# Optimization experiments

Hardware: AMD Instinct MI355X
Metric: run time of the kernel (lower is better)

The kernel has to match this reference:

```python
import jax, jax.numpy as jnp
import numpy as np
from jax import lax

FI, FO, K, EPS = 512, 256, 3, 1e-06


def _fir_kernel(gain):
    f = jnp.array([1.0, 3.0, 3.0, 1.0], dtype=jnp.float32)
    f = f[None, :] * f[:, None]
    f = f / f.sum() * gain  # (4,4), symmetric so conv-vs-correlation flip is a no-op
    return f


def setup_inputs() -> dict:
    key = jax.random.key(0)
    k1, k2 = jax.random.split(key)
    x = jax.random.normal(k1, (8, FI, 64, 64), dtype=jnp.float32)
    w = jax.random.normal(k2, (1, FO, FI, K, K), dtype=jnp.float32)
    return {"x": x, "w": w}


def reference(x, w):
    w_scale = (FI * K * K) ** (-0.5)
    wm = w[0] * w_scale  # (fo, fi, k, k); per-sample scale is constant across batch
    demod = lax.rsqrt(jnp.sum(wm * wm, axis=(1, 2, 3)) + EPS)  # (fo,)
    wm = wm * demod[:, None, None, None]
    # torch conv_transpose2d(stride=2, padding=0) with weight (fi, fo, k, k) where
    # weight[i, o] = wm[o, i]  ==  dilated conv with kernel flip(wm) OIHW, pad k-1=2.
    kern = wm[:, :, ::-1, ::-1]
    y = lax.conv_general_dilated(
        x, kern, window_strides=(1, 1), padding=[(2, 2), (2, 2)],
        lhs_dilation=(2, 2), dimension_numbers=("NCHW", "OIHW", "NCHW"))
    # upFirDn2D with scale=2, conv_k=3: p=0 -> pad (1,1) both dims, filter gain 4
    f = _fir_kernel(4.0)
    C = y.shape[1]
    fk = jnp.broadcast_to(f[None, None], (C, 1, 4, 4))
    y = lax.conv_general_dilated(
        y, fk, window_strides=(1, 1), padding=[(1, 1), (1, 1)],
        feature_group_count=C, dimension_numbers=("NCHW", "OIHW", "NCHW"))
    return y  # (8, 256, 128, 128)
```

## Files before the change

kernel.cpp:

```cpp
#include <hip/hip_runtime.h>

typedef unsigned short u16;
typedef unsigned int u32;
typedef __attribute__((ext_vector_type(8))) short bf16x8;
typedef __attribute__((ext_vector_type(4))) float f32x4;

#define XP_BYTES 35684352
#define YB_BYTES 68714544
#define HY_OFF   (XP_BYTES + YB_BYTES)
#define WS_NEED  ((size_t)HY_OFF + 2359296)
#define CS 16776

__device__ inline u16 f2bf(float f) {
  union { float f; unsigned u; } v; v.f = f;
  unsigned r = v.u + 0x7fffu + ((v.u >> 16) & 1u);
  return (u16)(r >> 16);
}

__device__ inline void gl_lds16(const u16* g, u16* l) {
  __builtin_amdgcn_global_load_lds(
      (const __attribute__((address_space(1))) unsigned int*)g,
      (__attribute__((address_space(3))) unsigned int*)l, 16, 0, 0);
}

__global__ void xprep(const float* __restrict__ x, u16* __restrict__ xp) {
  __shared__ float tile[64 * 65];
  int bid = blockIdx.x;
  int cc = bid & 7, h = (bid >> 3) & 63, n = bid >> 9;
  int c0 = cc * 64;
  int t = threadIdx.x;
  const float* xb = x + ((size_t)(n * 512 + c0) * 64 + h) * 64;
  for (int r = 0; r < 16; ++r) {
    int flat = r * 256 + t;
    int ci = flat >> 6, w = flat & 63;
    tile[w * 65 + ci] = xb[(size_t)ci * 4096 + w];
  }
  __syncthreads();
  for (int r = 0; r < 8; ++r) {
    int flat = r * 256 + t;
    int pr = flat & 31;
    int w = flat >> 5;
    int ci = pr * 2;
    float v0 = tile[w * 65 + ci], v1 = tile[w * 65 + ci + 1];
    unsigned pk = (unsigned)f2bf(v0) | ((unsigned)f2bf(v1) << 16);
    int kcabs = cc * 2 + (ci >> 5);
    int chl = ci & 31;
    u16* dst = xp + (size_t)(n * 16 + kcabs) * 139392 +
               (size_t)((h + 1) * 66 + (w + 1)) * 32 + chl;
    *(unsigned*)dst = pk;
  }
  if (t < 64) {
    int seg = t >> 4;
    int colsel = (seg >> 1) ? 65 : 0;
    int pl = cc * 2 + (seg & 1);
    int ui = t & 15;
    u16* dst = xp + (size_t)(n * 16 + pl) * 139392 +
               (size_t)((h + 1) * 66 + colsel) * 32 + ui * 2;
    *(u32*)dst = 0u;
  }
  if (h == 0 || h == 63) {
    int rowbase = (h == 0) ? 0 : 65 * 66;
    for (int j = t; j < 2112; j += 256) {
      int seg = j >> 4;
      int ui = j & 15;
      int pl = cc * 2 + (seg & 1);
      int pos = seg >> 1;
      u16* dst = xp + (size_t)(n * 16 + pl) * 139392 +
                 (size_t)(rowbase + pos) * 32 + ui * 2;
      *(u32*)dst = 0u;
    }
  }
}

__global__ void wprep9(const float* __restrict__ w, u16* __restrict__ Hy) {
  __shared__ float wl[4608];
  __shared__ float red[256];
  int o = blockIdx.x, t = threadIdx.x;
  const float* wo = w + (size_t)o * 4608;
  float s = 0.f;
  for (int j = t; j < 4608; j += 256) { float v = wo[j]; wl[j] = v; s += v * v; }
  red[t] = s;
  __syncthreads();
  for (int st = 128; st; st >>= 1) { if (t < st) red[t] += red[t + st]; __syncthreads(); }
  float demod = rsqrtf(red[0] * (1.0f / 4608.0f) + 1e-6f);
  float scale = demod * 0.014731391274719739f;
  const int DY[9] = {0, 2, 0, 2, 0, 2, 1, 1, 1};
  const int DX[9] = {0, 0, 2, 2, 1, 1, 0, 2, 1};
  for (int i = t; i < 512; i += 256) {
    int kc = i >> 5, il = i & 31;
#pragma unroll
    for (int pl = 0; pl < 9; ++pl) {
      float g = wl[i * 9 + DY[pl] * 3 + DX[pl]] * scale;
      Hy[(size_t)(pl * 16 + kc) * 8192 + (size_t)o * 32 + il] = f2bf(g);
    }
  }
}

#define BARR() __builtin_amdgcn_s_barrier()
#define WAITL() do { asm volatile("s_waitcnt lgkmcnt(0)" ::: "memory"); __builtin_amdgcn_sched_barrier(0); } while (0)
#define WAITV1() do { asm volatile("s_waitcnt vmcnt(1)" ::: "memory"); __builtin_amdgcn_sched_barrier(0); } while (0)
#define WAITV0() do { asm volatile("s_waitcnt vmcnt(0)" ::: "memory"); __builtin_amdgcn_sched_barrier(0); } while (0)

__device__ __forceinline__ void rdA4(const u16* sbA, int la, int grp, int hi,
                                     bf16x8 af[4]) {
#pragma unroll
  for (int ti = 0; ti < 4; ++ti) {
    int p = ti * 16 + la;
    int slot = (hi * 4 + grp) ^ (p & 7);
    af[ti] = *(const bf16x8*)(sbA + p * 64 + slot * 8);
  }
}

__device__ __forceinline__ bf16x8 rdB1(const u16* sb, int r, int grp) {
  int p = r & 63, hi = r >> 6;
  int slot = (hi * 4 + grp) ^ (p & 7);
  return *(const bf16x8*)(sb + 8192 + p * 64 + slot * 8);
}

template <int MI, int NI>
__device__ __forceinline__ void qmfma4(const bf16x8 af[4], bf16x8 bf,
                                       f32x4 acc[8][2]) {
#pragma unroll
  for (int ti = 0; ti < 4; ++ti)
    acc[MI * 4 + ti][NI] = __builtin_amdgcn_mfma_f32_16x16x32_bf16(
        af[ti], bf, acc[MI * 4 + ti][NI], 0, 0, 0);
}

__device__ __forceinline__ void stA1(const u16* __restrict__ xp, u16* d,
                                     int tile, int NK, u32 a,
                                     u32 adj1, u32 adj2, u32 adj3) {
  if (tile < NK) {
    int tap = tile >> 4;
    u32 ko = (u32)((tile & 15) * 139392);
    u32 adj = tap == 0 ? 0u : (tap == 1 ? adj1 : (tap == 2 ? adj2 : adj3));
    gl_lds16(xp + (a + ko - adj), d);
  }
}

__device__ __forceinline__ void stB1(const u16* __restrict__ hb, u16* d,
                                     int tile, int NK, u32 b) {
  if (tile < NK) {
    int tap = tile >> 4;
    u32 ko = (u32)(tap * 131072 + (tile & 15) * 8192);
    gl_lds16(hb + (b + ko), d);
  }
}

__global__ __launch_bounds__(512, 4) void conv_y(const u16* __restrict__ xp,
                                                 const u16* __restrict__ Hy,
                                                 u16* __restrict__ yb) {
  __shared__ __align__(16) u16 su[24576];

  int bid = blockIdx.x;
  int t = threadIdx.x;
  int wid = t >> 6, lane = t & 63;

  int img = bid & 7;
  int kk = bid >> 3;
  int mt, oh, Wp, CNT, NTAP, PB, PO, STLIM;
  u32 adj1 = 0, adj2 = 0, adj3 = 0;
  if (kk < 34)       { int k2 = kk;       mt = k2 >> 1; oh = k2 & 1; Wp = 66; CNT = 4290; NTAP = 4; PB = 0; PO = 0;     STLIM = 4296;
                       adj1 = 2112u; adj2 = 32u; adj3 = 2144u; }
  else if (kk < 68)  { int k2 = kk - 34;  mt = k2 >> 1; oh = k2 & 1; Wp = 64; CNT = 4160; NTAP = 2; PB = 4; PO = 4296;  STLIM = 4160;
                       adj1 = 2112u; }
  else if (kk < 102) { int k2 = kk - 68;  mt = k2 >> 1; oh = k2 & 1; Wp = 66; CNT = 4224; NTAP = 2; PB = 6; PO = 8456;  STLIM = 4224;
                       adj1 = 32u; }
  else               { int k2 = kk - 102; mt = k2 >> 1; oh = k2 & 1; Wp = 64; CNT = 4096; NTAP = 1; PB = 8; PO = 12680; STLIM = 4096; }

  int m0 = mt * 256;
  int o0 = oh * 128;
  int NK = NTAP * 16;
  int NITER = NTAP * 8;
  const u16* hb = Hy + (size_t)PB * 131072;

  int wm = wid >> 2, wn = wid & 3;
  int la = lane & 15, grp = lane >> 4;

  int sp = t >> 3;
  int se = (t & 7) ^ (sp & 7);
  int shi = se >> 2, sc = se & 3;
  int sloc = shi * 64 + sp;

  u32 gA0, gA1, gB;
  {
    u32 ib = (u32)img * 2230272u;
    int m = m0 + sloc;
    if (m > CNT - 1) m = CNT - 1;
    u32 a = (u32)m / (u32)Wp;
    u32 b = (u32)m - a * (u32)Wp;
    gA0 = ib + ((a + 1) * 66 + (b + 1)) * 32 + sc * 8;
    m = m0 + 128 + sloc;
    if (m > CNT - 1) m = CNT - 1;
    a = (u32)m / (u32)Wp;
    b = (u32)m - a * (u32)Wp;
    gA1 = ib + ((a + 1) * 66 + (b + 1)) * 32 + sc * 8;
    gB = (u32)((o0 + sloc) * 32 + sc * 8);
  }
  int ws = wid * 512;

  f32x4 acc[8][2];
#pragma unroll
  for (int i = 0; i < 8; ++i)
#pragma unroll
    for (int j = 0; j < 2; ++j) acc[i][j] = (f32x4){0.f, 0.f, 0.f, 0.f};

  stB1(hb, su + 8192 + ws, 0, NK, gB);
  stA1(xp, su + 0 + ws, 0, NK, gA0, adj1, adj2, adj3);
  stA1(xp, su + 4096 + ws, 0, NK, gA1, adj1, adj2, adj3);
  stB1(hb, su + 20480 + ws, 1, NK, gB);
  WAITV1();
  BARR();

  bf16x8 af[4], bf0, bf1;

#pragma unroll 1
  for (int it = 0; it < NITER; ++it) {
    int t0 = 2 * it;
    bool more = (it + 1 < NITER);

    rdA4(su + wm * 4096, la, grp, 0, af);
    bf0 = rdB1(su, wn * 32 + la, grp);
    stA1(xp, su + 12288 + ws, t0 + 1, NK, gA0, adj1, adj2, adj3);
    BARR(); WAITL();
    __builtin_amdgcn_s_setprio(1); qmfma4<0, 0>(af, bf0, acc); __builtin_amdgcn_s_setprio(0);
    BARR();
    bf1 = rdB1(su, wn * 32 + 16 + la, grp);
    stA1(xp, su + 16384 + ws, t0 + 1, NK, gA1, adj1, adj2, adj3);
    BARR(); WAITL();
    __builtin_amdgcn_s_setprio(1); qmfma4<0, 1>(af, bf1, acc); __builtin_amdgcn_s_setprio(0);
    BARR();
    rdA4(su + wm * 4096, la, grp, 1, af);
    stB1(hb, su + 8192 + ws, t0 + 2, NK, gB);
    BARR(); WAITL();
    __builtin_amdgcn_s_setprio(1);
    qmfma4<1, 1>(af, bf1, acc); qmfma4<1, 0>(af, bf0, acc);
    __builtin_amdgcn_s_setprio(0);
    if (more) { WAITV1(); } else { WAITV0(); }
    BARR();
    rdA4(su + 12288 + wm * 4096, la, grp, 0, af);
    bf0 = rdB1(su + 12288, wn * 32 + la, grp);
    stA1(xp, su + 0 + ws, t0 + 2, NK, gA0, adj1, adj2, adj3);
    BARR(); WAITL();
    __builtin_amdgcn_s_setprio(1); qmfma4<0, 0>(af, bf0, acc); __builtin_amdgcn_s_setprio(0);
    BARR();
    bf1 = rdB1(su + 12288, wn * 32 + 16 + la, grp);
    stA1(xp, su + 4096 + ws, t0 + 2, NK, gA1, adj1, adj2, adj3);
    BARR(); WAITL();
    __builtin_amdgcn_s_setprio(1); qmfma4<0, 1>(af, bf1, acc); __builtin_amdgcn_s_setprio(0);
    BARR();
    rdA4(su + 12288 + wm * 4096, la, grp, 1, af);
    stB1(hb, su + 20480 + ws, t0 + 3, NK, gB);
    BARR(); WAITL();
    __builtin_amdgcn_s_setprio(1);
    qmfma4<1, 1>(af, bf1, acc); qmfma4<1, 0>(af, bf0, acc);
    __builtin_amdgcn_s_setprio(0);
    if (more) { WAITV1(); }
    BARR();
  }

  WAITV0();
  __syncthreads();
  u16* ybp = yb + 8;
#pragma unroll 1
  for (int r = 0; r < 2; ++r) {
    if ((wn >> 1) == r) {
      int base_orl = (wn & 1) * 32;
#pragma unroll
      for (int nj = 0; nj < 2; ++nj) {
        int orl = base_orl + nj * 16 + la;
        int x7 = orl & 7;
#pragma unroll
        for (int mi8 = 0; mi8 < 8; ++mi8)
#pragma unroll
          for (int jp = 0; jp < 2; ++jp) {
            int ml = wm * 128 + mi8 * 16 + grp * 4 + jp * 2;
            u32 pk = (u32)f2bf(acc[mi8][nj][jp * 2]) |
                     ((u32)f2bf(acc[mi8][nj][jp * 2 + 1]) << 16);
            *(u32*)(su + orl * 256 + (((ml >> 3) ^ x7) * 8) + (ml & 7)) = pk;
          }
      }
    }
    __syncthreads();
    {
      int ol = t >> 3, s2 = t & 7;
      int og = o0 + r * 64 + ol;
      size_t gb = (size_t)(img * 256 + og) * CS + PO + m0;
      int x7 = ol & 7;
#pragma unroll
      for (int i = 0; i < 4; ++i) {
        int cidx = s2 * 4 + i;
        int m = cidx * 8;
        if (m0 + m < STLIM)
          *(bf16x8*)(ybp + gb + m) = *(const bf16x8*)(su + ol * 256 + ((cidx ^ x7) * 8));
      }
    }
    if (r == 0) __syncthreads();
  }
}

__global__ void fir2(const u16* __restrict__ yb, float* __restrict__ z) {
  int flat = blockIdx.x * 256 + threadIdx.x;
  int qh = flat & 15, phb = (flat >> 4) & 31, o = (flat >> 9) & 255, n = flat >> 17;
  const u16* cb = yb + 8 + (size_t)(n * 256 + o) * CS;
  int a0 = 2 * phb - 1;
  int b0 = 4 * qh - 1;

  float out[4][8];
#pragma unroll
  for (int i = 0; i < 4; ++i)
#pragma unroll
    for (int j = 0; j < 8; ++j) out[i][j] = 0.f;

  const int PO_[4] = {0, 4296, 8456, 12680};
  const int WP_[4] = {66, 64, 66, 64};
  const int HA_[4] = {65, 65, 64, 64};
  const int WB_[4] = {65, 64, 65, 64};

#pragma unroll
  for (int ph = 0; ph < 4; ++ph) {
    int rp = ph >> 1, rq = ph & 1;
    const u16* pb = cb + PO_[ph];
    float hcol[4][8];
#pragma unroll
    for (int la = 0; la < 4; ++la) {
      if (rp == 0 && la == 0) continue;
      int ag = a0 + la;
      bool rv = (ag >= 0) && (ag < HA_[ph]);
      const u16* rb = pb + (ag * WP_[ph] + b0 - 1);
      u32 ls[4];
      ls[0] = *(const u32*)(rb);
      ls[1] = *(const u32*)(rb + 2);
      ls[2] = *(const u32*)(rb + 4);
      ls[3] = *(const u32*)(rb + 6);
      float v[6];
#pragma unroll
      for (int lb = 0; lb < 6; ++lb) {
        int jj = lb + 1;
        u32 w16 = (jj & 1) ? (ls[jj >> 1] >> 16) : (ls[jj >> 1] & 0xffffu);
        float fv = __uint_as_float(w16 << 16);
        int bg = b0 + lb;
        bool ok = rv && (bg >= 0) && (bg < WB_[ph]);
        v[lb] = ok ? fv : 0.f;
      }
#pragma unroll
      for (int e = 0; e < 4; ++e) {
        if (rq == 0) {
          hcol[la][2 * e]     = 3.f * v[e + 1] + v[e + 2];
          hcol[la][2 * e + 1] = v[e + 1] + 3.f * v[e + 2];
        } else {
          hcol[la][2 * e]     = v[e] + 3.f * v[e + 1];
          hcol[la][2 * e + 1] = 3.f * v[e + 1] + v[e + 2];
        }
      }
    }
#pragma unroll
    for (int jq = 0; jq < 8; ++jq) {
      if (rp == 0) {
        out[0][jq] += 3.f * hcol[1][jq] + hcol[2][jq];
        out[1][jq] += hcol[1][jq] + 3.f * hcol[2][jq];
        out[2][jq] += 3.f * hcol[2][jq] + hcol[3][jq];
        out[3][jq] += hcol[2][jq] + 3.f * hcol[3][jq];
      } else {
        out[0][jq] += hcol[0][jq] + 3.f * hcol[1][jq];
        out[1][jq] += 3.f * hcol[1][jq] + hcol[2][jq];
        out[2][jq] += hcol[1][jq] + 3.f * hcol[2][jq];
        out[3][jq] += 3.f * hcol[2][jq] + hcol[3][jq];
      }
    }
  }

  float* zb = z + ((size_t)(n * 256 + o) * 128 + phb * 4) * 128 + qh * 8;
#pragma unroll
  for (int ip = 0; ip < 4; ++ip) {
    f32x4 v0, v1;
#pragma unroll
    for (int j = 0; j < 4; ++j) { v0[j] = out[ip][j] * 0.0625f; v1[j] = out[ip][j + 4] * 0.0625f; }
    *(f32x4*)(zb + (size_t)ip * 128) = v0;
    *(f32x4*)(zb + (size_t)ip * 128 + 4) = v1;
  }
}

__global__ void xprep_flat(const float* __restrict__ x, u16* __restrict__ xp) {
  __shared__ float tile[64 * 65];
  int bid = blockIdx.x;
  int cc = bid & 7, h = (bid >> 3) & 63, n = bid >> 9;
  int c0 = cc * 64;
  int t = threadIdx.x;
  const float* xb = x + ((size_t)(n * 512 + c0) * 64 + h) * 64;
  for (int r = 0; r < 16; ++r) {
    int flat = r * 256 + t;
    int ci = flat >> 6, w = flat & 63;
    tile[w * 65 + ci] = xb[(size_t)ci * 4096 + w];
  }
  __syncthreads();
  u16* xpb = xp + ((size_t)(n * 66 + h + 1) * 66 + 1) * 512 + c0;
  for (int r = 0; r < 8; ++r) {
    int flat = r * 256 + t;
    int pr = flat & 31;
    int w = flat >> 5;
    int ci = pr * 2;
    float v0 = tile[w * 65 + ci], v1 = tile[w * 65 + ci + 1];
    unsigned pk = (unsigned)f2bf(v0) | ((unsigned)f2bf(v1) << 16);
    *(unsigned*)(xpb + (size_t)w * 512 + ci) = pk;
  }
  u16* rowbase = xp + ((size_t)(n * 66 + h + 1) * 66) * 512 + c0;
  if (t < 32) *(u32*)(rowbase + 2 * t) = 0u;
  else if (t < 64) *(u32*)(rowbase + (size_t)65 * 512 + 2 * (t - 32)) = 0u;
  if (h == 0) {
    u16* r0 = xp + ((size_t)(n * 66) * 66) * 512 + c0;
    for (int j = t; j < 2112; j += 256) {
      int col = j >> 5, wi = j & 31;
      *(u32*)(r0 + (size_t)col * 512 + 2 * wi) = 0u;
    }
  }
  if (h == 63) {
    u16* r65 = xp + ((size_t)(n * 66 + 65) * 66) * 512 + c0;
    for (int j = t; j < 2112; j += 256) {
      int col = j >> 5, wi = j & 31;
      *(u32*)(r65 + (size_t)col * 512 + 2 * wi) = 0u;
    }
  }
}

__global__ void wprep36(const float* __restrict__ w, u16* __restrict__ Hm) {
  __shared__ float wl[4608];
  __shared__ float red[256];
  int o = blockIdx.x, t = threadIdx.x;
  const float* wo = w + (size_t)o * 4608;
  float s = 0.f;
  for (int j = t; j < 4608; j += 256) { float v = wo[j]; wl[j] = v; s += v * v; }
  red[t] = s;
  __syncthreads();
  for (int st = 128; st; st >>= 1) { if (t < st) red[t] += red[t + st]; __syncthreads(); }
  float demod = rsqrtf(red[0] * (1.0f / 4608.0f) + 1e-6f);
  float scale = demod * 0.014731391274719739f;
  const float F1[4] = {1.f, 3.f, 3.f, 1.f};
  for (int i = t; i < 512; i += 256) {
    float wm[9];
    for (int k = 0; k < 9; ++k) wm[k] = wl[i * 9 + k] * scale;
    for (int rp = 0; rp < 2; ++rp)
      for (int rq = 0; rq < 2; ++rq)
        for (int u = 0; u < 3; ++u)
          for (int v = 0; v < 3; ++v) {
            int s_ = 2 - 2 * u + rp, t_ = 2 - 2 * v + rq;
            float g = 0.f;
            for (int dy = 0; dy < 3; ++dy) {
              int a = dy + 1 - s_;
              if (a < 0 || a > 3) continue;
              for (int dx = 0; dx < 3; ++dx) {
                int b = dx + 1 - t_;
                if (b < 0 || b > 3) continue;
                g += wm[dy * 3 + dx] * (F1[a] * F1[b]);
              }
            }
            g *= 0.0625f;
            Hm[(size_t)((rp * 2 + rq) * 9 + u * 3 + v) * 131072 + (size_t)o * 512 + i] = f2bf(g);
          }
  }
}

__global__ __launch_bounds__(256) void conv_main(const u16* __restrict__ xp,
                                                 const u16* __restrict__ Hm,
                                                 float* __restrict__ z) {
  __shared__ __align__(16) float smemf[8448];
  u16* su = (u16*)smemf;
  int bid = blockIdx.x;
  int sub = bid & 7;
  int rp = sub >> 2;
  int o0 = (sub & 3) * 64;
  int mtile = bid >> 3;
  int n_img = mtile >> 5;
  int hp0 = (mtile & 31) * 2;
  int t = threadIdx.x;
  int wave = t >> 6, lane = t & 63;
  int wm0 = (wave & 1) * 64;
  int wn0 = (wave >> 1) * 32;
  int la = lane & 15;
  int ks = (lane >> 4) * 8;
  int rsel = t >> 2;
  int koff = (t & 3) * 8;
  f32x4 acc[2][4][2];
#pragma unroll
  for (int a = 0; a < 2; ++a)
#pragma unroll
    for (int b = 0; b < 4; ++b)
#pragma unroll
      for (int c = 0; c < 2; ++c)
        acc[a][b][c] = (f32x4){0.f, 0.f, 0.f, 0.f};
#pragma unroll 1
  for (int tap = 0; tap < 9; ++tap) {
    int du = tap / 3, dv = tap - du * 3;
    const u16* gA0 = xp + ((size_t)(n_img * 66 + hp0 + du) * 66 + dv) * 512;
    const u16* gB0 = Hm + (size_t)(rp * 18 + tap) * 131072 + (size_t)(o0 + rsel) * 512 + koff;
    const u16* gAr0 = gA0 + (size_t)rsel * 512 + koff;
    const u16* gAr1 = gA0 + (size_t)(66 + rsel) * 512 + koff;
#pragma unroll 1
    for (int kc = 0; kc < 16; ++kc) {
      int c0 = kc * 32;
      __syncthreads();
      gl_lds16(gAr0 + c0, su + wave * 512);
      gl_lds16(gAr1 + c0, su + 2048 + wave * 512);
      gl_lds16(gB0 + c0,              su + 4096 + wave * 512);
      gl_lds16(gB0 + 9 * 131072 + c0, su + 6144 + wave * 512);
      __syncthreads();
      bf16x8 af[4];
#pragma unroll
      for (int ti = 0; ti < 4; ++ti)
        af[ti] = *(const bf16x8*)(su + (wm0 + ti * 16 + la) * 32 + ks);
      bf16x8 bfr[2][2];
#pragma unroll
      for (int rqq = 0; rqq < 2; ++rqq)
#pragma unroll
        for (int tj = 0; tj < 2; ++tj)
          bfr[rqq][tj] = *(const bf16x8*)(su + 4096 + rqq * 2048 + (wn0 + tj * 16 + la) * 32 + ks);
#pragma unroll
      for (int rqq = 0; rqq < 2; ++rqq)
#pragma unroll
        for (int ti = 0; ti < 4; ++ti)
#pragma unroll
          for (int tj = 0; tj < 2; ++tj)
            acc[rqq][ti][tj] = __builtin_amdgcn_mfma_f32_16x16x32_bf16(
                af[ti], bfr[rqq][tj], acc[rqq][ti][tj], 0, 0, 0);
    }
  }
  __syncthreads();
  float* lws = smemf + wave * 2112;
  int p = 2 * (hp0 + (wave & 1)) + rp;
#pragma unroll
  for (int tj = 0; tj < 2; ++tj) {
#pragma unroll
    for (int rqq = 0; rqq < 2; ++rqq)
#pragma unroll
      for (int ti = 0; ti < 4; ++ti) {
        int wqb = ti * 16 + (lane >> 4) * 4;
        f32x4 v = acc[rqq][ti][tj];
#pragma unroll
        for (int r = 0; r < 4; ++r)
          lws[la * 132 + 2 * (wqb + r) + rqq] = v[r];
      }
    __syncthreads();
    int obase = o0 + wn0 + tj * 16;
#pragma unroll
    for (int c = 0; c < 8; ++c) {
      int idx = c * 64 + lane;
      int ol = idx >> 5, q4 = (idx & 31) * 4;
      f32x4 vv = *(const f32x4*)(lws + ol * 132 + q4);
      *(f32x4*)(z + (((size_t)n_img * 256 + obase + ol) * 128 + p) * 128 + q4) = vv;
    }
    __syncthreads();
  }
}

extern "C" void kernel_launch(void* const* d_in, const int* in_sizes, int n_in,
                              void* d_out, int out_size, void* d_ws, size_t ws_size,
                              hipStream_t stream) {
  const float* x = (const float*)d_in[0];
  const float* w = (const float*)d_in[1];
  float* z = (float*)d_out;
  u16* xp = (u16*)d_ws;

  if (ws_size >= WS_NEED) {
    u16* yb = (u16*)((char*)d_ws + XP_BYTES);
    u16* hy = (u16*)((char*)d_ws + HY_OFF);
    xprep<<<4096, 256, 0, stream>>>(x, xp);
    wprep9<<<256, 256, 0, stream>>>(w, hy);
    conv_y<<<1072, 512, 0, stream>>>(xp, hy, yb);
    fir2<<<4096, 256, 0, stream>>>(yb, z);
  } else {
    u16* Hm = (u16*)((char*)d_ws + XP_BYTES);
    hipMemsetAsync(xp, 0, XP_BYTES, stream);
    xprep_flat<<<4096, 256, 0, stream>>>(x, xp);
    wprep36<<<256, 256, 0, stream>>>(w, Hm);
    conv_main<<<2048, 256, 0, stream>>>(xp, Hm, z);
  }
}
```

Before: 311.6 us.

## Halve conv block to 256 threads with larger per-wave 128x64 MFMA tiles

The implicit-GEMM conv kernel moves from 512 threads (8 waves, 128x32 per wave) to 256 threads (4 waves, 128x64 per wave), with each thread issuing twice as many async global-to-LDS loads per stage. Each wave now reuses its A fragments across four N sub-tiles, which cuts LDS reads per MFMA, and the vmcnt waits and epilogue store mapping are adjusted to match. In exchange, accumulator registers double and the launch bound drops to 2 blocks per SM, so fewer waves are available to hide latency.

New measurement: 312.6 us. No clear change (+0.3%).

```diff
diff --git a/kernel.cpp b/kernel.cpp
--- a/kernel.cpp
+++ b/kernel.cpp
@@ -98,32 +98,38 @@
 
 #define BARR() __builtin_amdgcn_s_barrier()
 #define WAITL() do { asm volatile("s_waitcnt lgkmcnt(0)" ::: "memory"); __builtin_amdgcn_sched_barrier(0); } while (0)
-#define WAITV1() do { asm volatile("s_waitcnt vmcnt(1)" ::: "memory"); __builtin_amdgcn_sched_barrier(0); } while (0)
+#define WAITV2() do { asm volatile("s_waitcnt vmcnt(2)" ::: "memory"); __builtin_amdgcn_sched_barrier(0); } while (0)
 #define WAITV0() do { asm volatile("s_waitcnt vmcnt(0)" ::: "memory"); __builtin_amdgcn_sched_barrier(0); } while (0)
 
-__device__ __forceinline__ void rdA4(const u16* sbA, int la, int grp, int hi,
+__device__ __forceinline__ void rdA4(const u16* sb, int tib, int la, int grp, int wm,
                                      bf16x8 af[4]) {
 #pragma unroll
   for (int ti = 0; ti < 4; ++ti) {
-    int p = ti * 16 + la;
-    int slot = (hi * 4 + grp) ^ (p & 7);
-    af[ti] = *(const bf16x8*)(sbA + p * 64 + slot * 8);
-  }
-}
-
-__device__ __forceinline__ bf16x8 rdB1(const u16* sb, int r, int grp) {
-  int p = r & 63, hi = r >> 6;
-  int slot = (hi * 4 + grp) ^ (p & 7);
-  return *(const bf16x8*)(sb + 8192 + p * 64 + slot * 8);
-}
-
-template <int MI, int NI>
-__device__ __forceinline__ void qmfma4(const bf16x8 af[4], bf16x8 bf,
-                                       f32x4 acc[8][2]) {
+    int p = (tib + ti) * 16 + la;
+    int slot = (wm * 4 + grp) ^ (p & 7);
+    af[ti] = *(const bf16x8*)(sb + p * 64 + slot * 8);
+  }
+}
+
+__device__ __forceinline__ void rdB2(const u16* sb, int njb, int la, int grp, int wn,
+                                     bf16x8 bf[2]) {
+#pragma unroll
+  for (int nj = 0; nj < 2; ++nj) {
+    int p = (njb + nj) * 16 + la;
+    int slot = (wn * 4 + grp) ^ (p & 7);
+    bf[nj] = *(const bf16x8*)(sb + 8192 + p * 64 + slot * 8);
+  }
+}
+
+template <int MIB, int NJ0>
+__device__ __forceinline__ void qm8(const bf16x8 af[4], const bf16x8 bf[2],
+                                    f32x4 acc[8][4]) {
 #pragma unroll
   for (int ti = 0; ti < 4; ++ti)
-    acc[MI * 4 + ti][NI] = __builtin_amdgcn_mfma_f32_16x16x32_bf16(
-        af[ti], bf, acc[MI * 4 + ti][NI], 0, 0, 0);
+#pragma unroll
+    for (int nj = 0; nj < 2; ++nj)
+      acc[MIB + ti][NJ0 + nj] = __builtin_amdgcn_mfma_f32_16x16x32_bf16(
+          af[ti], bf[nj], acc[MIB + ti][NJ0 + nj], 0, 0, 0);
 }
 
 __device__ __forceinline__ void stA1(const u16* __restrict__ xp, u16* d,
@@ -146,7 +152,7 @@
   }
 }
 
-__global__ __launch_bounds__(512, 4) void conv_y(const u16* __restrict__ xp,
+__global__ __launch_bounds__(256, 2) void conv_y(const u16* __restrict__ xp,
                                                  const u16* __restrict__ Hy,
                                                  u16* __restrict__ yb) {
   __shared__ __align__(16) u16 su[24576];
@@ -173,88 +179,103 @@
   int NITER = NTAP * 8;
   const u16* hb = Hy + (size_t)PB * 131072;
 
-  int wm = wid >> 2, wn = wid & 3;
+  int wm = wid >> 1, wn = wid & 1;
   int la = lane & 15, grp = lane >> 4;
 
-  int sp = t >> 3;
-  int se = (t & 7) ^ (sp & 7);
-  int shi = se >> 2, sc = se & 3;
-  int sloc = shi * 64 + sp;
-
-  u32 gA0, gA1, gB;
+  int tp = t >> 3, ts = t & 7;
+  u32 gA[4], gBv[2];
   {
     u32 ib = (u32)img * 2230272u;
-    int m = m0 + sloc;
-    if (m > CNT - 1) m = CNT - 1;
-    u32 a = (u32)m / (u32)Wp;
-    u32 b = (u32)m - a * (u32)Wp;
-    gA0 = ib + ((a + 1) * 66 + (b + 1)) * 32 + sc * 8;
-    m = m0 + 128 + sloc;
-    if (m > CNT - 1) m = CNT - 1;
-    a = (u32)m / (u32)Wp;
-    b = (u32)m - a * (u32)Wp;
-    gA1 = ib + ((a + 1) * 66 + (b + 1)) * 32 + sc * 8;
-    gB = (u32)((o0 + sloc) * 32 + sc * 8);
+#pragma unroll
+    for (int j = 0; j < 4; ++j) {
+      int p = j * 32 + tp;
+      int e = ts ^ (p & 7);
+      int ii = (e >> 2) * 128 + p;
+      int kc = e & 3;
+      int m = m0 + ii;
+      if (m > CNT - 1) m = CNT - 1;
+      u32 a = (u32)m / (u32)Wp;
+      u32 b = (u32)m - a * (u32)Wp;
+      gA[j] = ib + ((a + 1) * 66 + (b + 1)) * 32 + kc * 8;
+    }
+#pragma unroll
+    for (int j = 0; j < 2; ++j) {
+      int p = j * 32 + tp;
+      int e = ts ^ (p & 7);
+      int ol = (e >> 2) * 64 + p;
+      int kc = e & 3;
+      gBv[j] = (u32)((o0 + ol) * 32 + kc * 8);
+    }
   }
   int ws = wid * 512;
 
-  f32x4 acc[8][2];
+  f32x4 acc[8][4];
 #pragma unroll
   for (int i = 0; i < 8; ++i)
 #pragma unroll
-    for (int j = 0; j < 2; ++j) acc[i][j] = (f32x4){0.f, 0.f, 0.f, 0.f};
-
-  stB1(hb, su + 8192 + ws, 0, NK, gB);
-  stA1(xp, su + 0 + ws, 0, NK, gA0, adj1, adj2, adj3);
-  stA1(xp, su + 4096 + ws, 0, NK, gA1, adj1, adj2, adj3);
-  stB1(hb, su + 20480 + ws, 1, NK, gB);
-  WAITV1();
+    for (int j = 0; j < 4; ++j) acc[i][j] = (f32x4){0.f, 0.f, 0.f, 0.f};
+
+  stB1(hb, su + 8192 + ws, 0, NK, gBv[0]);
+  stB1(hb, su + 10240 + ws, 0, NK, gBv[1]);
+  stA1(xp, su + 0 + ws, 0, NK, gA[0], adj1, adj2, adj3);
+  stA1(xp, su + 2048 + ws, 0, NK, gA[1], adj1, adj2, adj3);
+  stA1(xp, su + 4096 + ws, 0, NK, gA[2], adj1, adj2, adj3);
+  stA1(xp, su + 6144 + ws, 0, NK, gA[3], adj1, adj2, adj3);
+  stB1(hb, su + 20480 + ws, 1, NK, gBv[0]);
+  stB1(hb, su + 22528 + ws, 1, NK, gBv[1]);
+  WAITV2();
   BARR();
 
-  bf16x8 af[4], bf0, bf1;
+  bf16x8 afA[4], afB[4], bfA[2], bfB[2];
 
 #pragma unroll 1
   for (int it = 0; it < NITER; ++it) {
     int t0 = 2 * it;
     bool more = (it + 1 < NITER);
 
-    rdA4(su + wm * 4096, la, grp, 0, af);
-    bf0 = rdB1(su, wn * 32 + la, grp);
-    stA1(xp, su + 12288 + ws, t0 + 1, NK, gA0, adj1, adj2, adj3);
+    rdA4(su, 0, la, grp, wm, afA);
+    rdB2(su, 0, la, grp, wn, bfA);
+    stA1(xp, su + 12288 + ws, t0 + 1, NK, gA[0], adj1, adj2, adj3);
+    stA1(xp, su + 14336 + ws, t0 + 1, NK, gA[1], adj1, adj2, adj3);
     BARR(); WAITL();
-    __builtin_amdgcn_s_setprio(1); qmfma4<0, 0>(af, bf0, acc); __builtin_amdgcn_s_setprio(0);
+    __builtin_amdgcn_s_setprio(1); qm8<0, 0>(afA, bfA, acc); __builtin_amdgcn_s_setprio(0);
     BARR();
-    bf1 = rdB1(su, wn * 32 + 16 + la, grp);
-    stA1(xp, su + 16384 + ws, t0 + 1, NK, gA1, adj1, adj2, adj3);
+    rdB2(su, 2, la, grp, wn, bfB);
+    stA1(xp, su + 16384 + ws, t0 + 1, NK, gA[2], adj1, adj2, adj3);
+    stA1(xp, su + 18432 + ws, t0 + 1, NK, gA[3], adj1, adj2, adj3);
     BARR(); WAITL();
-    __builtin_amdgcn_s_setprio(1); qmfma4<0, 1>(af, bf1, acc); __builtin_amdgcn_s_setprio(0);
+    __builtin_amdgcn_s_setprio(1); qm8<0, 2>(afA, bfB, acc); __builtin_amdgcn_s_setprio(0);
     BARR();
-    rdA4(su + wm * 4096, la, grp, 1, af);
-    stB1(hb, su + 8192 + ws, t0 + 2, NK, gB);
+    rdA4(su, 4, la, grp, wm, afB);
+    stB1(hb, su + 8192 + ws, t0 + 2, NK, gBv[0]);
+    stB1(hb, su + 10240 + ws, t0 + 2, NK, gBv[1]);
     BARR(); WAITL();
     __builtin_amdgcn_s_setprio(1);
-    qmfma4<1, 1>(af, bf1, acc); qmfma4<1, 0>(af, bf0, acc);
+    qm8<4, 0>(afB, bfA, acc); qm8<4, 2>(afB, bfB, acc);
     __builtin_amdgcn_s_setprio(0);
-    if (more) { WAITV1(); } else { WAITV0(); }
+    if (more) { WAITV2(); } else { WAITV0(); }
     BARR();
-    rdA4(su + 12288 + wm * 4096, la, grp, 0, af);
-    bf0 = rdB1(su + 12288, wn * 32 + la, grp);
-    stA1(xp, su + 0 + ws, t0 + 2, NK, gA0, adj1, adj2, adj3);
+    rdA4(su + 12288, 0, la, grp, wm, afA);
+    rdB2(su + 12288, 0, la, grp, wn, bfA);
+    stA1(xp, su + 0 + ws, t0 + 2, NK, gA[0], adj1, adj2, adj3);
+    stA1(xp, su + 2048 + ws, t0 + 2, NK, gA[1], adj1, adj2, adj3);
     BARR(); WAITL();
-    __builtin_amdgcn_s_setprio(1); qmfma4<0, 0>(af, bf0, acc); __builtin_amdgcn_s_setprio(0);
+    __builtin_amdgcn_s_setprio(1); qm8<0, 0>(afA, bfA, acc); __builtin_amdgcn_s_setprio(0);
     BARR();
-    bf1 = rdB1(su + 12288, wn * 32 + 16 + la, grp);
-    stA1(xp, su + 4096 + ws, t0 + 2, NK, gA1, adj1, adj2, adj3);
+    rdB2(su + 12288, 2, la, grp, wn, bfB);
+    stA1(xp, su + 4096 + ws, t0 + 2, NK, gA[2], adj1, adj2, adj3);
+    stA1(xp, su + 6144 + ws, t0 + 2, NK, gA[3], adj1, adj2, adj3);
     BARR(); WAITL();
-    __builtin_amdgcn_s_setprio(1); qmfma4<0, 1>(af, bf1, acc); __builtin_amdgcn_s_setprio(0);
+    __builtin_amdgcn_s_setprio(1); qm8<0, 2>(afA, bfB, acc); __builtin_amdgcn_s_setprio(0);
     BARR();
-    rdA4(su + 12288 + wm * 4096, la, grp, 1, af);
-    stB1(hb, su + 20480 + ws, t0 + 3, NK, gB);
+    rdA4(su + 12288, 4, la, grp, wm, afB);
+    stB1(hb, su + 20480 + ws, t0 + 3, NK, gBv[0]);
+    stB1(hb, su + 22528 + ws, t0 + 3, NK, gBv[1]);
     BARR(); WAITL();
     __builtin_amdgcn_s_setprio(1);
-    qmfma4<1, 1>(af, bf1, acc); qmfma4<1, 0>(af, bf0, acc);
+    qm8<4, 0>(afB, bfA, acc); qm8<4, 2>(afB, bfB, acc);
     __builtin_amdgcn_s_setprio(0);
-    if (more) { WAITV1(); }
+    if (more) { WAITV2(); }
     BARR();
   }
 
@@ -263,32 +284,31 @@
   u16* ybp = yb + 8;
 #pragma unroll 1
   for (int r = 0; r < 2; ++r) {
-    if ((wn >> 1) == r) {
-      int base_orl = (wn & 1) * 32;
-#pragma unroll
-      for (int nj = 0; nj < 2; ++nj) {
-        int orl = base_orl + nj * 16 + la;
+    if (wn == r) {
+#pragma unroll
+      for (int nj = 0; nj < 4; ++nj) {
+        int orl = nj * 16 + la;
         int x7 = orl & 7;
 #pragma unroll
-        for (int mi8 = 0; mi8 < 8; ++mi8)
+        for (int mi = 0; mi < 8; ++mi)
 #pragma unroll
           for (int jp = 0; jp < 2; ++jp) {
-            int ml = wm * 128 + mi8 * 16 + grp * 4 + jp * 2;
-            u32 pk = (u32)f2bf(acc[mi8][nj][jp * 2]) |
-                     ((u32)f2bf(acc[mi8][nj][jp * 2 + 1]) << 16);
+            int ml = wm * 128 + mi * 16 + grp * 4 + jp * 2;
+            u32 pk = (u32)f2bf(acc[mi][nj][jp * 2]) |
+                     ((u32)f2bf(acc[mi][nj][jp * 2 + 1]) << 16);
             *(u32*)(su + orl * 256 + (((ml >> 3) ^ x7) * 8) + (ml & 7)) = pk;
           }
       }
     }
     __syncthreads();
     {
-      int ol = t >> 3, s2 = t & 7;
+      int ol = t >> 2, s2 = t & 3;
       int og = o0 + r * 64 + ol;
       size_t gb = (size_t)(img * 256 + og) * CS + PO + m0;
       int x7 = ol & 7;
 #pragma unroll
-      for (int i = 0; i < 4; ++i) {
-        int cidx = s2 * 4 + i;
+      for (int i = 0; i < 8; ++i) {
+        int cidx = s2 * 8 + i;
         int m = cidx * 8;
         if (m0 + m < STLIM)
           *(bf16x8*)(ybp + gb + m) = *(const bf16x8*)(su + ol * 256 + ((cidx ^ x7) * 8));
@@ -564,7 +584,7 @@
     u16* hy = (u16*)((char*)d_ws + HY_OFF);
     xprep<<<4096, 256, 0, stream>>>(x, xp);
     wprep9<<<256, 256, 0, stream>>>(w, hy);
-    conv_y<<<1072, 512, 0, stream>>>(xp, hy, yb);
+    conv_y<<<1072, 256, 0, stream>>>(xp, hy, yb);
     fir2<<<4096, 256, 0, stream>>>(yb, z);
   } else {
     u16* Hm = (u16*)((char*)d_ws + XP_BYTES);
```
